# Performance work log

Measured on AMD Instinct MI355X. Metric: run time of the kernel, lower is better.

## Reference

```python
import jax, jax.numpy as jnp
import numpy as np

B, T, C = 4, 2048, 1024
H = 16
DH = C // H  # 64


def setup_inputs() -> dict:
    key = jax.random.key(0)
    ks = jax.random.split(key, 6)
    s = 1.0 / np.sqrt(C)
    x = jax.random.normal(ks[0], (B, T, C), dtype=jnp.float32)
    # per-head projection weights, stacked: (H, C, DH)
    Wq = jax.random.uniform(ks[1], (H, C, DH), dtype=jnp.float32, minval=-s, maxval=s)
    Wk = jax.random.uniform(ks[2], (H, C, DH), dtype=jnp.float32, minval=-s, maxval=s)
    Wv = jax.random.uniform(ks[3], (H, C, DH), dtype=jnp.float32, minval=-s, maxval=s)
    # output projection (torch Linear: y = x @ W.T + b); store as (C, C) for x @ Wo
    Wo = jax.random.uniform(ks[4], (C, C), dtype=jnp.float32, minval=-s, maxval=s)
    bo = jax.random.uniform(ks[5], (C,), dtype=jnp.float32, minval=-s, maxval=s)
    return {"x": x, "Wq": Wq, "Wk": Wk, "Wv": Wv, "Wo": Wo, "bo": bo}


def reference(x, Wq, Wk, Wv, Wo, bo):
    # x: (B,T,C) -> q,k,v: (B,H,T,DH)
    q = jnp.einsum('btc,hcd->bhtd', x, Wq)
    k = jnp.einsum('btc,hcd->bhtd', x, Wk)
    v = jnp.einsum('btc,hcd->bhtd', x, Wv)
    scale = DH ** -0.5
    scores = jnp.einsum('bhtd,bhsd->bhts', q, k) * scale  # (B,H,T,T)
    causal = jnp.tril(jnp.ones((T, T), dtype=bool))
    scores = jnp.where(causal, scores, -jnp.inf)
    wei = jax.nn.softmax(scores, axis=-1)
    out = jnp.einsum('bhts,bhsd->bhtd', wei, v)  # (B,H,T,DH)
    # concat heads: (B,T,H*DH) = (B,T,C)
    out = out.transpose(0, 2, 1, 3).reshape(B, T, C)
    return out @ Wo + bo
```

## Files before the change

### kernel.cpp

```cpp
#include <hip/hip_runtime.h>

#define T_SEQ 2048
#define C_DIM 1024
#define H_NUM 16
#define DHD   64
#define B_NUM 4
#define M_ROWS (B_NUM*T_SEQ)

typedef __bf16 bf16x8 __attribute__((ext_vector_type(8)));
typedef float  f32x4  __attribute__((ext_vector_type(4)));
typedef unsigned short ushort8 __attribute__((ext_vector_type(8)));
typedef unsigned short ushort4e __attribute__((ext_vector_type(4)));

__device__ __forceinline__ unsigned short f2b(float f){
  return __builtin_bit_cast(unsigned short, (__bf16)f);
}
__device__ __forceinline__ bf16x8 as_bf(ushort8 u){ return __builtin_bit_cast(bf16x8, u); }
__device__ __forceinline__ float exp2fast(float x){ return __builtin_amdgcn_exp2f(x); }

__device__ __forceinline__ void gload16(const void* g, void* l){
  __builtin_amdgcn_global_load_lds(
      (const __attribute__((address_space(1))) void*)g,
      (__attribute__((address_space(3))) void*)l, 16, 0, 0);
}

#define MF(a,b,c) __builtin_amdgcn_mfma_f32_16x16x32_bf16(a,b,c,0,0,0)

__global__ __launch_bounds__(256) void k_prep(const float* __restrict__ x,
                                              const float* __restrict__ wq,
                                              const float* __restrict__ wk,
                                              const float* __restrict__ wv,
                                              const float* __restrict__ wo,
                                              unsigned short* __restrict__ xb,
                                              unsigned short* __restrict__ wt,
                                              unsigned short* __restrict__ wot){
  const int bid = blockIdx.x;
  if (bid < 8192){
    int i = bid*256 + threadIdx.x;
    float4 f = ((const float4*)x)[i];
    ushort4e o;
    o[0]=f2b(f.x); o[1]=f2b(f.y); o[2]=f2b(f.z); o[3]=f2b(f.w);
    ((ushort4e*)xb)[i] = o;
  } else {
    int idx = (bid - 8192)*256 + threadIdx.x;
    if (idx < 3*C_DIM*C_DIM){
      int nall = idx >> 10; int c = idx & 1023;
      int m = nall >> 10;   int n = nall & 1023;
      int h = n >> 6, d = n & 63;
      const float* w = (m==0) ? wq : (m==1) ? wk : wv;
      float f = w[((size_t)h*C_DIM + c)*DHD + d];
      if (m == 0) f *= 0.125f * 1.4426950408889634f;
      wt[idx] = f2b(f);
    } else {
      int j = idx - 3*C_DIM*C_DIM;
      int n = j >> 10, c = j & 1023;
      wot[j] = f2b(wo[(size_t)c*C_DIM + n]);
    }
  }
}

__global__ __launch_bounds__(256) void k_gemm_qkv(const unsigned short* __restrict__ xb,
                                                  const unsigned short* __restrict__ wt,
                                                  unsigned short* __restrict__ qo,
                                                  unsigned short* __restrict__ ko,
                                                  unsigned short* __restrict__ vtr){
  __shared__ __align__(16) unsigned short smem[2][128*64];
  const int tid = threadIdx.x, lane = tid & 63, wid = tid >> 6;
  const int g = lane >> 4, tl = lane & 15;
  const int wr = wid >> 1, wc = wid & 1;
  const int id = blockIdx.x;
  const int xcd = id & 7, i = id >> 3;
  const int xm = xcd >> 1, xn = xcd & 1;
  const int mbase = (xm*16 + i/12) * 128, nbase = (xn*12 + i%12) * 128;
  f32x4 acc[4][4] = {};
  for (int kk = 0; kk < C_DIM; kk += 64){
    __syncthreads();
    #pragma unroll
    for (int i2 = 0; i2 < 4; i2++){
      const int brow = (wid*4 + i2)*8;
      const int row  = brow + (lane >> 3);
      const int jj   = (lane & 7) ^ (row & 7);
      gload16(&xb[(size_t)(mbase+row)*C_DIM + kk + jj*8], &smem[0][brow*64]);
      gload16(&wt[(size_t)(nbase+row)*C_DIM + kk + jj*8], &smem[1][brow*64]);
    }
    __syncthreads();
    bf16x8 aF[4][2], bF[4][2];
    #pragma unroll
    for (int mb = 0; mb < 4; mb++){
      const int row = wr*64 + mb*16 + tl; const int s7 = row & 7;
      aF[mb][0] = as_bf(*(const ushort8*)&smem[0][row*64 + ((g     ^ s7)*8)]);
      aF[mb][1] = as_bf(*(const ushort8*)&smem[0][row*64 + (((4+g) ^ s7)*8)]);
    }
    #pragma unroll
    for (int nb = 0; nb < 4; nb++){
      const int row = wc*64 + nb*16 + tl; const int s7 = row & 7;
      bF[nb][0] = as_bf(*(const ushort8*)&smem[1][row*64 + ((g     ^ s7)*8)]);
      bF[nb][1] = as_bf(*(const ushort8*)&smem[1][row*64 + (((4+g) ^ s7)*8)]);
    }
    #pragma unroll
    for (int mb = 0; mb < 4; mb++)
      #pragma unroll
      for (int nb = 0; nb < 4; nb++){
        acc[mb][nb] = MF(aF[mb][0], bF[nb][0], acc[mb][nb]);
        acc[mb][nb] = MF(aF[mb][1], bF[nb][1], acc[mb][nb]);
      }
  }
  const int sel = nbase >> 10;
  if (sel < 2){
    unsigned short* dst0 = (sel == 0) ? qo : ko;
    #pragma unroll
    for (int mb = 0; mb < 4; mb++){
      #pragma unroll
      for (int nb = 0; nb < 4; nb++){
        #pragma unroll
        for (int r = 0; r < 4; r++){
          int gr = mbase + wr*64 + mb*16 + g*4 + r;
          int gc = nbase + wc*64 + nb*16 + tl;
          int b = gr >> 11, t = gr & 2047;
          int nw = gc & 1023;
          int h = nw >> 6, d = nw & 63;
          dst0[(((size_t)(b*H_NUM + h))*T_SEQ + t)*DHD + d] = f2b(acc[mb][nb][r]);
        }
      }
    }
  } else {
    __syncthreads();
    unsigned short* tr = &smem[0][0];
    #pragma unroll
    for (int mb = 0; mb < 4; mb++){
      #pragma unroll
      for (int nb = 0; nb < 4; nb++){
        const int n = wc*64 + nb*16 + tl;
        const int m0 = wr*64 + mb*16 + g*4;
        ushort4e pk;
        #pragma unroll
        for (int r = 0; r < 4; r++) pk[r] = f2b(acc[mb][nb][r]);
        *(ushort4e*)&tr[n*128 + (m0 ^ ((n & 15) << 3))] = pk;
      }
    }
    __syncthreads();
    const int hbase = (nbase - 2048) >> 6;
    const int b = mbase >> 11, tloc = mbase & 2047;
    const int n = tid >> 1, half = tid & 1;
    unsigned short* vdst = vtr + (((size_t)(b*H_NUM + hbase + (n >> 6)))*DHD + (n & 63))*T_SEQ
                           + tloc + half*64;
    const int nx = (n & 15) << 3;
    #pragma unroll
    for (int c8 = 0; c8 < 8; c8++){
      const int t0 = half*64 + (c8 >> 2)*32 + (c8 & 3)*4;
      ushort4e lo = *(const ushort4e*)&tr[n*128 + ((t0     ) ^ nx)];
      ushort4e hi = *(const ushort4e*)&tr[n*128 + ((t0 + 16) ^ nx)];
      ushort8 u;
      #pragma unroll
      for (int e = 0; e < 4; e++){ u[e] = lo[e]; u[4+e] = hi[e]; }
      *(ushort8*)&vdst[c8*8] = u;
    }
  }
}

__global__ __launch_bounds__(512) void k_flash(const unsigned short* __restrict__ q,
                                               const unsigned short* __restrict__ k,
                                               const unsigned short* __restrict__ vtg,
                                               unsigned short* __restrict__ o){
  __shared__ __align__(16) unsigned short kbufs[2][64*64];
  __shared__ __align__(16) unsigned short vbufs[2][64*64];
  const int tid = threadIdx.x, lane = tid & 63, w = tid >> 6;
  const int g = lane >> 4, tl = lane & 15;
  const int id = blockIdx.x;
  const int swz = (id & 7)*32 + (id >> 3);
  const int bh = swz >> 2, bx = swz & 3;
  const int b = bh >> 4, h = bh & 15;
  const unsigned short* qb = q   + (size_t)bh * T_SEQ * DHD;
  const unsigned short* kb = k   + (size_t)bh * T_SEQ * DHD;
  const unsigned short* vb = vtg + (size_t)bh * (size_t)DHD * T_SEQ;
  const int lrow = lane >> 3, lj = lane & 7;

  for (int pass = 0; pass < 2; ++pass){
    const int qt = pass ? (7 - bx) : bx;
    const int tbase = qt * 256;
    const int trow0 = tbase + w * 32;
    const int tmax = trow0 + 31;
    bf16x8 qF[2][2];
    #pragma unroll
    for (int tf = 0; tf < 2; tf++)
      #pragma unroll
      for (int ks = 0; ks < 2; ks++)
        qF[tf][ks] = as_bf(*(const ushort8*)&qb[(size_t)(trow0 + tf*16 + tl)*DHD + ks*32 + g*8]);
    f32x4 acc[2][4] = {};
    float mreg[2] = {-1e30f, -1e30f}, lreg[2] = {0.f, 0.f};
    const int nkt = 4*qt + 4;
    {
      const int row = w*8 + lrow;
      const int jj = lj ^ (row & 7);
      gload16(&kb[(size_t)row*DHD + jj*8],   &kbufs[0][w*8*64]);
      gload16(&vb[(size_t)row*T_SEQ + jj*8], &vbufs[0][w*8*64]);
    }
    __syncthreads();
    for (int kti = 0; kti < nkt; ++kti){
      const int cur = kti & 1;
      const int kbase = kti * 64;
      if (kti + 1 < nkt){
        const int kb2 = kbase + 64;
        const int row = w*8 + lrow;
        const int jj = lj ^ (row & 7);
        gload16(&kb[(size_t)(kb2+row)*DHD + jj*8],   &kbufs[cur^1][w*8*64]);
        gload16(&vb[(size_t)row*T_SEQ + kb2 + jj*8], &vbufs[cur^1][w*8*64]);
      }
      if (kbase <= tmax){
        const unsigned short* kcur = kbufs[cur];
        const unsigned short* vcur = vbufs[cur];
        const int s7 = tl & 7;
        f32x4 st[2][4] = {};
        __builtin_amdgcn_s_setprio(1);
        #pragma unroll
        for (int sf = 0; sf < 4; sf++){
          const int row = sf*16 + tl;
          bf16x8 kf0 = as_bf(*(const ushort8*)&kcur[row*64 + ((g     ^ s7)*8)]);
          bf16x8 kf1 = as_bf(*(const ushort8*)&kcur[row*64 + (((4+g) ^ s7)*8)]);
          #pragma unroll
          for (int tf = 0; tf < 2; tf++){
            st[tf][sf] = MF(kf0, qF[tf][0], st[tf][sf]);
            st[tf][sf] = MF(kf1, qF[tf][1], st[tf][sf]);
          }
        }
        __builtin_amdgcn_s_setprio(0);
        if (kbase + 63 > trow0){
          #pragma unroll
          for (int tf = 0; tf < 2; tf++){
            int tg = trow0 + tf*16 + tl;
            #pragma unroll
            for (int sf = 0; sf < 4; sf++)
              #pragma unroll
              for (int r = 0; r < 4; r++)
                if (kbase + sf*16 + g*4 + r > tg) st[tf][sf][r] = -1e30f;
          }
        }
        #pragma unroll
        for (int tf = 0; tf < 2; tf++){
          float mloc = -1e30f;
          #pragma unroll
          for (int sf = 0; sf < 4; sf++)
            #pragma unroll
            for (int r = 0; r < 4; r++) mloc = fmaxf(mloc, st[tf][sf][r]);
          if (__any(mloc > mreg[tf] + 8.f)){
            float mrow = fmaxf(mloc, __shfl_xor(mloc, 16));
            mrow = fmaxf(mrow, __shfl_xor(mrow, 32));
            float mnew = fmaxf(mreg[tf], mrow);
            float alpha = exp2fast(mreg[tf] - mnew);
            mreg[tf] = mnew;
            lreg[tf] *= alpha;
            #pragma unroll
            for (int df = 0; df < 4; df++)
              #pragma unroll
              for (int r = 0; r < 4; r++) acc[tf][df][r] *= alpha;
          }
          float sum = 0.f;
          #pragma unroll
          for (int sf = 0; sf < 4; sf++)
            #pragma unroll
            for (int r = 0; r < 4; r++){
              float p = exp2fast(st[tf][sf][r] - mreg[tf]);
              sum += p;
              st[tf][sf][r] = p;
            }
          lreg[tf] += sum;
        }
        bf16x8 pa[2][2];
        #pragma unroll
        for (int tf = 0; tf < 2; tf++)
          #pragma unroll
          for (int ks = 0; ks < 2; ks++){
            ushort8 u;
            #pragma unroll
            for (int r = 0; r < 4; r++){
              u[r]   = f2b(st[tf][2*ks  ][r]);
              u[4+r] = f2b(st[tf][2*ks+1][r]);
            }
            pa[tf][ks] = as_bf(u);
          }
        __builtin_amdgcn_s_setprio(1);
        #pragma unroll
        for (int df = 0; df < 4; df++){
          const int row = df*16 + tl;
          bf16x8 vfr[2];
          #pragma unroll
          for (int ks = 0; ks < 2; ks++)
            vfr[ks] = as_bf(*(const ushort8*)&vcur[row*64 + (((4*ks + g) ^ s7)*8)]);
          #pragma unroll
          for (int tf = 0; tf < 2; tf++){
            acc[tf][df] = MF(vfr[0], pa[tf][0], acc[tf][df]);
            acc[tf][df] = MF(vfr[1], pa[tf][1], acc[tf][df]);
          }
        }
        __builtin_amdgcn_s_setprio(0);
      }
      __syncthreads();
    }
    #pragma unroll
    for (int tf = 0; tf < 2; tf++){
      float l = lreg[tf];
      l += __shfl_xor(l, 16);
      l += __shfl_xor(l, 32);
      float inv = 1.f / l;
      int tg = trow0 + tf*16 + tl;
      #pragma unroll
      for (int df = 0; df < 4; df++){
        ushort4e ov;
        #pragma unroll
        for (int r = 0; r < 4; r++) ov[r] = f2b(acc[tf][df][r] * inv);
        *(ushort4e*)&o[((size_t)(b*T_SEQ + tg))*C_DIM + h*DHD + df*16 + g*4] = ov;
      }
    }
  }
}

__global__ __launch_bounds__(256) void k_gemm_proj(const unsigned short* __restrict__ ab,
                                                   const unsigned short* __restrict__ wot,
                                                   const float* __restrict__ bo,
                                                   float* __restrict__ out){
  __shared__ __align__(16) unsigned short a_lds[128*64];
  __shared__ __align__(16) unsigned short b_lds[128*64];
  const int tid = threadIdx.x, lane = tid & 63, wid = tid >> 6;
  const int g = lane >> 4, tl = lane & 15;
  const int wr = wid >> 1, wc = wid & 1;
  const int id = blockIdx.x;
  const int swz = (id & 7)*64 + (id >> 3);
  const int mbase = (swz >> 3) * 128, nbase = (swz & 7) * 128;
  f32x4 acc[4][4] = {};
  for (int kk = 0; kk < C_DIM; kk += 64){
    __syncthreads();
    #pragma unroll
    for (int i = 0; i < 4; i++){
      const int brow = (wid*4 + i)*8;
      const int row  = brow + (lane >> 3);
      const int jj   = (lane & 7) ^ (row & 7);
      gload16(&ab[(size_t)(mbase+row)*C_DIM + kk + jj*8],  &a_lds[brow*64]);
      gload16(&wot[(size_t)(nbase+row)*C_DIM + kk + jj*8], &b_lds[brow*64]);
    }
    __syncthreads();
    bf16x8 aF[4][2], bF[4][2];
    #pragma unroll
    for (int mb = 0; mb < 4; mb++){
      const int row = wr*64 + mb*16 + tl; const int s7 = row & 7;
      aF[mb][0] = as_bf(*(const ushort8*)&a_lds[row*64 + ((g     ^ s7)*8)]);
      aF[mb][1] = as_bf(*(const ushort8*)&a_lds[row*64 + (((4+g) ^ s7)*8)]);
    }
    #pragma unroll
    for (int nb = 0; nb < 4; nb++){
      const int row = wc*64 + nb*16 + tl; const int s7 = row & 7;
      bF[nb][0] = as_bf(*(const ushort8*)&b_lds[row*64 + ((g     ^ s7)*8)]);
      bF[nb][1] = as_bf(*(const ushort8*)&b_lds[row*64 + (((4+g) ^ s7)*8)]);
    }
    #pragma unroll
    for (int mb = 0; mb < 4; mb++)
      #pragma unroll
      for (int nb = 0; nb < 4; nb++){
        acc[mb][nb] = MF(aF[mb][0], bF[nb][0], acc[mb][nb]);
        acc[mb][nb] = MF(aF[mb][1], bF[nb][1], acc[mb][nb]);
      }
  }
  #pragma unroll
  for (int mb = 0; mb < 4; mb++){
    #pragma unroll
    for (int nb = 0; nb < 4; nb++){
      #pragma unroll
      for (int r = 0; r < 4; r++){
        int gr = mbase + wr*64 + mb*16 + g*4 + r;
        int gc = nbase + wc*64 + nb*16 + tl;
        out[(size_t)gr*C_DIM + gc] = acc[mb][nb][r] + bo[gc];
      }
    }
  }
}

extern "C" void kernel_launch(void* const* d_in, const int* in_sizes, int n_in,
                              void* d_out, int out_size, void* d_ws, size_t ws_size,
                              hipStream_t stream){
  const float* x  = (const float*)d_in[0];
  const float* Wq = (const float*)d_in[1];
  const float* Wk = (const float*)d_in[2];
  const float* Wv = (const float*)d_in[3];
  const float* Wo = (const float*)d_in[4];
  const float* bo = (const float*)d_in[5];
  float* out = (float*)d_out;

  char* p = (char*)d_ws;
  unsigned short* xb  = (unsigned short*)p; p += (size_t)M_ROWS*C_DIM*2;
  unsigned short* wt  = (unsigned short*)p; p += (size_t)3*C_DIM*C_DIM*2;
  unsigned short* wot = (unsigned short*)p; p += (size_t)C_DIM*C_DIM*2;
  unsigned short* Qb  = (unsigned short*)p; p += (size_t)M_ROWS*C_DIM*2;
  unsigned short* Kb  = (unsigned short*)p; p += (size_t)M_ROWS*C_DIM*2;
  unsigned short* Vtr = (unsigned short*)p; p += (size_t)M_ROWS*C_DIM*2;
  unsigned short* attn = xb;

  hipLaunchKernelGGL(k_prep, dim3(8192 + 16384), dim3(256), 0, stream,
                     x, Wq, Wk, Wv, Wo, xb, wt, wot);
  hipLaunchKernelGGL(k_gemm_qkv, dim3(1536), dim3(256), 0, stream,
                     xb, wt, Qb, Kb, Vtr);
  hipLaunchKernelGGL(k_flash, dim3(256), dim3(512), 0, stream,
                     Qb, Kb, Vtr, attn);
  hipLaunchKernelGGL(k_gemm_proj, dim3(512), dim3(256), 0, stream,
                     attn, wot, bo, out);
}
```

Baseline: 177.1 us.

## Give each flash-attention wave 64 query rows with 4 waves per block

```diff
diff --git a/kernel.cpp b/kernel.cpp
--- a/kernel.cpp
+++ b/kernel.cpp
@@ -158,7 +158,7 @@
   }
 }
 
-__global__ __launch_bounds__(512) void k_flash(const unsigned short* __restrict__ q,
+__global__ __launch_bounds__(256) void k_flash(const unsigned short* __restrict__ q,
                                                const unsigned short* __restrict__ k,
                                                const unsigned short* __restrict__ vtg,
                                                unsigned short* __restrict__ o){
@@ -174,26 +174,30 @@
   const unsigned short* kb = k   + (size_t)bh * T_SEQ * DHD;
   const unsigned short* vb = vtg + (size_t)bh * (size_t)DHD * T_SEQ;
   const int lrow = lane >> 3, lj = lane & 7;
+  const int s7 = tl & 7;
 
   for (int pass = 0; pass < 2; ++pass){
     const int qt = pass ? (7 - bx) : bx;
     const int tbase = qt * 256;
-    const int trow0 = tbase + w * 32;
-    const int tmax = trow0 + 31;
-    bf16x8 qF[2][2];
-    #pragma unroll
-    for (int tf = 0; tf < 2; tf++)
+    const int trow0 = tbase + w * 64;
+    const int tmax = trow0 + 63;
+    bf16x8 qF[4][2];
+    #pragma unroll
+    for (int tf = 0; tf < 4; tf++)
       #pragma unroll
       for (int ks = 0; ks < 2; ks++)
         qF[tf][ks] = as_bf(*(const ushort8*)&qb[(size_t)(trow0 + tf*16 + tl)*DHD + ks*32 + g*8]);
-    f32x4 acc[2][4] = {};
-    float mreg[2] = {-1e30f, -1e30f}, lreg[2] = {0.f, 0.f};
+    f32x4 acc[4][4] = {};
+    float mreg[4], lreg[4];
+    #pragma unroll
+    for (int tf = 0; tf < 4; tf++){ mreg[tf] = -1e30f; lreg[tf] = 0.f; }
     const int nkt = 4*qt + 4;
-    {
-      const int row = w*8 + lrow;
+    #pragma unroll
+    for (int i = 0; i < 2; i++){
+      const int row = w*16 + i*8 + lrow;
       const int jj = lj ^ (row & 7);
-      gload16(&kb[(size_t)row*DHD + jj*8],   &kbufs[0][w*8*64]);
-      gload16(&vb[(size_t)row*T_SEQ + jj*8], &vbufs[0][w*8*64]);
+      gload16(&kb[(size_t)row*DHD + jj*8],   &kbufs[0][(w*16 + i*8)*64]);
+      gload16(&vb[(size_t)row*T_SEQ + jj*8], &vbufs[0][(w*16 + i*8)*64]);
     }
     __syncthreads();
     for (int kti = 0; kti < nkt; ++kti){
@@ -201,16 +205,18 @@
       const int kbase = kti * 64;
       if (kti + 1 < nkt){
         const int kb2 = kbase + 64;
-        const int row = w*8 + lrow;
-        const int jj = lj ^ (row & 7);
-        gload16(&kb[(size_t)(kb2+row)*DHD + jj*8],   &kbufs[cur^1][w*8*64]);
-        gload16(&vb[(size_t)row*T_SEQ + kb2 + jj*8], &vbufs[cur^1][w*8*64]);
+        #pragma unroll
+        for (int i = 0; i < 2; i++){
+          const int row = w*16 + i*8 + lrow;
+          const int jj = lj ^ (row & 7);
+          gload16(&kb[(size_t)(kb2+row)*DHD + jj*8],   &kbufs[cur^1][(w*16 + i*8)*64]);
+          gload16(&vb[(size_t)row*T_SEQ + kb2 + jj*8], &vbufs[cur^1][(w*16 + i*8)*64]);
+        }
       }
       if (kbase <= tmax){
         const unsigned short* kcur = kbufs[cur];
         const unsigned short* vcur = vbufs[cur];
-        const int s7 = tl & 7;
-        f32x4 st[2][4] = {};
+        f32x4 st[4][4] = {};
         __builtin_amdgcn_s_setprio(1);
         #pragma unroll
         for (int sf = 0; sf < 4; sf++){
@@ -218,7 +224,7 @@
           bf16x8 kf0 = as_bf(*(const ushort8*)&kcur[row*64 + ((g     ^ s7)*8)]);
           bf16x8 kf1 = as_bf(*(const ushort8*)&kcur[row*64 + (((4+g) ^ s7)*8)]);
           #pragma unroll
-          for (int tf = 0; tf < 2; tf++){
+          for (int tf = 0; tf < 4; tf++){
             st[tf][sf] = MF(kf0, qF[tf][0], st[tf][sf]);
             st[tf][sf] = MF(kf1, qF[tf][1], st[tf][sf]);
           }
@@ -226,7 +232,7 @@
         __builtin_amdgcn_s_setprio(0);
         if (kbase + 63 > trow0){
           #pragma unroll
-          for (int tf = 0; tf < 2; tf++){
+          for (int tf = 0; tf < 4; tf++){
             int tg = trow0 + tf*16 + tl;
             #pragma unroll
             for (int sf = 0; sf < 4; sf++)
@@ -235,8 +241,9 @@
                 if (kbase + sf*16 + g*4 + r > tg) st[tf][sf][r] = -1e30f;
           }
         }
-        #pragma unroll
-        for (int tf = 0; tf < 2; tf++){
+        bf16x8 pa[4][2];
+        #pragma unroll
+        for (int tf = 0; tf < 4; tf++){
           float mloc = -1e30f;
           #pragma unroll
           for (int sf = 0; sf < 4; sf++)
@@ -256,28 +263,20 @@
           }
           float sum = 0.f;
           #pragma unroll
-          for (int sf = 0; sf < 4; sf++)
-            #pragma unroll
-            for (int r = 0; r < 4; r++){
-              float p = exp2fast(st[tf][sf][r] - mreg[tf]);
-              sum += p;
-              st[tf][sf][r] = p;
-            }
-          lreg[tf] += sum;
-        }
-        bf16x8 pa[2][2];
-        #pragma unroll
-        for (int tf = 0; tf < 2; tf++)
-          #pragma unroll
           for (int ks = 0; ks < 2; ks++){
             ushort8 u;
             #pragma unroll
             for (int r = 0; r < 4; r++){
-              u[r]   = f2b(st[tf][2*ks  ][r]);
-              u[4+r] = f2b(st[tf][2*ks+1][r]);
+              float p0 = exp2fast(st[tf][2*ks  ][r] - mreg[tf]);
+              float p1 = exp2fast(st[tf][2*ks+1][r] - mreg[tf]);
+              sum += p0 + p1;
+              u[r]   = f2b(p0);
+              u[4+r] = f2b(p1);
             }
             pa[tf][ks] = as_bf(u);
           }
+          lreg[tf] += sum;
+        }
         __builtin_amdgcn_s_setprio(1);
         #pragma unroll
         for (int df = 0; df < 4; df++){
@@ -287,7 +286,7 @@
           for (int ks = 0; ks < 2; ks++)
             vfr[ks] = as_bf(*(const ushort8*)&vcur[row*64 + (((4*ks + g) ^ s7)*8)]);
           #pragma unroll
-          for (int tf = 0; tf < 2; tf++){
+          for (int tf = 0; tf < 4; tf++){
             acc[tf][df] = MF(vfr[0], pa[tf][0], acc[tf][df]);
             acc[tf][df] = MF(vfr[1], pa[tf][1], acc[tf][df]);
           }
@@ -297,7 +296,7 @@
       __syncthreads();
     }
     #pragma unroll
-    for (int tf = 0; tf < 2; tf++){
+    for (int tf = 0; tf < 4; tf++){
       float l = lreg[tf];
       l += __shfl_xor(l, 16);
       l += __shfl_xor(l, 32);
@@ -397,7 +396,7 @@
                      x, Wq, Wk, Wv, Wo, xb, wt, wot);
   hipLaunchKernelGGL(k_gemm_qkv, dim3(1536), dim3(256), 0, stream,
                      xb, wt, Qb, Kb, Vtr);
-  hipLaunchKernelGGL(k_flash, dim3(256), dim3(512), 0, stream,
+  hipLaunchKernelGGL(k_flash, dim3(256), dim3(256), 0, stream,
                      Qb, Kb, Vtr, attn);
   hipLaunchKernelGGL(k_gemm_proj, dim3(512), dim3(256), 0, stream,
                      attn, wot, bo, out);
```

After: 196.6 us. +11.0%, slower.
